# Performance work log

Hardware: AMD Instinct MI355X
Metric: run time of the kernel (lower is better)

The kernel has to match this reference:

```python
import jax, jax.numpy as jnp
import numpy as np

B, L, D, H = 4, 2048, 1024, 16
HD = D // H  # head_dim = 64


def setup_inputs() -> dict:
    key = jax.random.key(0)
    k1, k2, k3 = jax.random.split(key, 3)
    scale_in = 1.0 / np.sqrt(D)
    return {
        "x": jax.random.normal(k1, (B, L, D), dtype=jnp.float32),
        "Wqkv": jax.random.normal(k2, (D, 3 * D), dtype=jnp.float32) * scale_in,
        "Wout": jax.random.normal(k3, (D, D), dtype=jnp.float32) * scale_in,
        "bout": jnp.zeros((D,), dtype=jnp.float32),
    }


def reference(x, Wqkv, Wout, bout):
    b, l, d = x.shape
    # QKV projection (no bias): [B, L, 3D] -> [B, L, 3, H, HD]
    qkv = (x @ Wqkv).reshape(b, l, 3, H, HD)
    q, k, v = jnp.moveaxis(qkv, 2, 0)  # each [B, L, H, HD]
    # scaled scores [B, H, L, L]
    scores = jnp.einsum("blhd,bmhd->bhlm", q, k) / jnp.sqrt(jnp.float32(HD))
    causal_mask = jnp.triu(jnp.ones((l, l), dtype=bool), k=1)
    scores = jnp.where(causal_mask, -jnp.inf, scores)
    attn = jax.nn.softmax(scores, axis=-1)
    # dropout p=0.0 (eval-mode reference) -> identity
    out = jnp.einsum("bhlm,bmhd->blhd", attn, v).reshape(b, l, d)
    return out @ Wout + bout
```

## Files before the change

### kernel.cpp

```cpp
#include <hip/hip_runtime.h>

typedef unsigned short ushort_t;
using bf16x8 = __attribute__((ext_vector_type(8))) short;
using f32x4  = __attribute__((ext_vector_type(4))) float;
using f32x16 = __attribute__((ext_vector_type(16))) float;
using u32x4  = __attribute__((ext_vector_type(4))) unsigned int;

#define B_  4
#define L_  2048
#define D_  1024
#define H_  16
#define HD_ 64
#define N3_ 3072
#define M1_ (B_ * L_)

static __device__ __forceinline__ unsigned short f2bf(float f) {
    unsigned int u = __float_as_uint(f);
    unsigned int r = (u + 0x7fffu + ((u >> 16) & 1u)) >> 16;
    return (unsigned short)r;
}

static __device__ __forceinline__ unsigned int pkbf(float lo, float hi) {
    unsigned int r;
    asm("v_cvt_pk_bf16_f32 %0, %1, %2" : "=v"(r) : "v"(lo), "v"(hi));
    return r;
}

static __device__ __forceinline__ void plswap(unsigned int& a, unsigned int& b) {
    asm volatile("v_permlane32_swap_b32 %0, %1" : "+v"(a), "+v"(b));
}

static __device__ __forceinline__ void async16(const void* g, const void* l) {
    __builtin_amdgcn_global_load_lds(
        (const __attribute__((address_space(1))) void*)g,
        (__attribute__((address_space(3))) void*)l, 16, 0, 0);
}

__global__ void convert_x_kernel(const float4* __restrict__ src,
                                 ushort4* __restrict__ dst) {
    int i = blockIdx.x * blockDim.x + threadIdx.x;
    float4 v = src[i];
    ushort4 o;
    o.x = f2bf(v.x); o.y = f2bf(v.y); o.z = f2bf(v.z); o.w = f2bf(v.w);
    dst[i] = o;
}

__global__ void transpose_conv_kernel(const float* __restrict__ src,
                                      unsigned short* __restrict__ dst,
                                      int rows, int cols) {
    __shared__ float tile[32][33];
    int tx = threadIdx.x, ty = threadIdx.y;
    int c0 = blockIdx.x * 32, r0 = blockIdx.y * 32;
    #pragma unroll
    for (int j = 0; j < 32; j += 8)
        tile[ty + j][tx] = src[(size_t)(r0 + ty + j) * cols + c0 + tx];
    __syncthreads();
    #pragma unroll
    for (int j = 0; j < 32; j += 8)
        dst[(size_t)(c0 + ty + j) * rows + r0 + tx] = f2bf(tile[tx][ty + j]);
}

__global__ __launch_bounds__(512, 2) void gemm256_qkv_kernel(
    const unsigned short* __restrict__ A, const unsigned short* __restrict__ BT,
    unsigned short* __restrict__ qb, unsigned short* __restrict__ kb,
    unsigned short* __restrict__ vb) {
    constexpr int K = 1024, BK = 32, NT = K / BK;
    constexpr int NBX = N3_ / 256;
    constexpr int NWG = (M1_ / 256) * NBX;
    __shared__ __align__(16) unsigned short lds[4][2][256 * BK];

    const int tid = threadIdx.x;
    const int w = tid >> 6, lane = tid & 63;
    const int wr = w >> 2, wc = w & 3;
    const int lg = lane >> 4, ll = lane & 15;

    const int bid = blockIdx.x;
    const int swz = (bid & 7) * (NWG / 8) + (bid >> 3);
    const int m0 = (swz / NBX) * 256, n0 = (swz % NBX) * 256;

    const int srow = w * 16 + (lane >> 2);
    const int scol = (lane & 3) * 8;

    f32x4 acc[8][4] = {};

    #pragma unroll 1
    for (int kt = -3; kt < NT; ++kt) {
        const int ks = kt + 3;
        if (ks < NT) {
            const int buf = ks & 3;
            const size_t koff = (size_t)ks * BK + scol;
            #pragma unroll
            for (int rd = 0; rd < 2; ++rd) {
                async16(&A[(size_t)(m0 + rd * 128 + srow) * K + koff],
                        &lds[buf][0][w * 512 + rd * 4096]);
                async16(&BT[(size_t)(n0 + rd * 128 + srow) * K + koff],
                        &lds[buf][1][w * 512 + rd * 4096]);
            }
        }
        if (kt < 0) continue;

        if (kt == 0) {
            asm volatile("s_waitcnt vmcnt(12)" ::: "memory");
        } else if (kt <= NT - 4) {
            asm volatile("s_waitcnt vmcnt(8)" ::: "memory");
        } else if (kt == NT - 3) {
            asm volatile("s_waitcnt vmcnt(4)" ::: "memory");
        } else {
            asm volatile("s_waitcnt vmcnt(0)" ::: "memory");
        }
        __builtin_amdgcn_s_barrier();
        __builtin_amdgcn_sched_barrier(0);

        const unsigned short* Ab = &lds[kt & 3][0][0];
        const unsigned short* Bb = &lds[kt & 3][1][0];
        bf16x8 af[8], bf[4];
        #pragma unroll
        for (int i = 0; i < 8; ++i)
            af[i] = *(const bf16x8*)&Ab[(wr * 128 + i * 16 + ll) * BK + lg * 8];
        #pragma unroll
        for (int j = 0; j < 4; ++j)
            bf[j] = *(const bf16x8*)&Bb[(wc * 64 + j * 16 + ll) * BK + lg * 8];

        __builtin_amdgcn_s_setprio(1);
        #pragma unroll
        for (int i = 0; i < 8; ++i)
            #pragma unroll
            for (int j = 0; j < 4; ++j)
                acc[i][j] = __builtin_amdgcn_mfma_f32_16x16x32_bf16(
                    af[i], bf[j], acc[i][j], 0, 0, 0);
        __builtin_amdgcn_s_setprio(0);
    }

    #pragma unroll
    for (int mi = 0; mi < 8; ++mi) {
        const int mb = m0 + wr * 128 + mi * 16 + lg * 4;
        #pragma unroll
        for (int ni = 0; ni < 4; ++ni) {
            const int n = n0 + wc * 64 + ni * 16 + ll;
            const int s = n >> 10, h = (n >> 6) & 15, hd = n & 63;
            if (s == 2) {
                const int b = mb >> 11, l = mb & 2047;
                const size_t base = (size_t)(b * H_ + h) * (L_ * HD_);
                ushort4 pk;
                pk.x = f2bf(acc[mi][ni][0]);
                pk.y = f2bf(acc[mi][ni][1]);
                pk.z = f2bf(acc[mi][ni][2]);
                pk.w = f2bf(acc[mi][ni][3]);
                *(ushort4*)&vb[base + (l >> 5) * 2048 + ((l >> 4) & 1) * 1024 +
                               ((l >> 3) & 1) * 512 + hd * 8 + (l & 7)] = pk;
            } else {
                #pragma unroll
                for (int r = 0; r < 4; ++r) {
                    const int m = mb + r;
                    const int b = m >> 11, l = m & 2047;
                    const size_t base = (size_t)(b * H_ + h) * (L_ * HD_);
                    const size_t o = base + (l >> 5) * 2048 + (hd >> 4) * 512 +
                                     ((hd >> 3) & 1) * 256 + (l & 31) * 8 + (hd & 7);
                    unsigned short bv = f2bf(acc[mi][ni][r]);
                    if (s == 0) qb[o] = bv; else kb[o] = bv;
                }
            }
        }
    }
}

__global__ __launch_bounds__(256) void gemm_bt_kernel(
    const unsigned short* __restrict__ A, const unsigned short* __restrict__ BT,
    float* __restrict__ outp, const float* __restrict__ bias) {
    constexpr int K = 1024;
    __shared__ unsigned short As[128 * 32];
    __shared__ unsigned short Bs[128 * 32];
    const int tid = threadIdx.x, w = tid >> 6, lane = tid & 63;
    const int m0 = blockIdx.y * 128, n0 = blockIdx.x * 128;
    const int wm = (w >> 1) * 64, wn = (w & 1) * 64;
    const int lg = lane >> 4, ll = lane & 15;

    f32x4 acc[4][4] = {};

    for (int k0 = 0; k0 < K; k0 += 32) {
        #pragma unroll
        for (int j = 0; j < 2; ++j) {
            int row = w * 32 + j * 16 + (lane >> 2);
            int col = (lane & 3) * 8;
            async16(&A[(size_t)(m0 + row) * K + k0 + col], &As[(w * 32 + j * 16) * 32]);
            async16(&BT[(size_t)(n0 + row) * K + k0 + col], &Bs[(w * 32 + j * 16) * 32]);
        }
        __syncthreads();
        bf16x8 af[4], bfr[4];
        #pragma unroll
        for (int i = 0; i < 4; ++i) {
            af[i]  = *(const bf16x8*)&As[(wm + i * 16 + ll) * 32 + lg * 8];
            bfr[i] = *(const bf16x8*)&Bs[(wn + i * 16 + ll) * 32 + lg * 8];
        }
        #pragma unroll
        for (int mi = 0; mi < 4; ++mi)
            #pragma unroll
            for (int ni = 0; ni < 4; ++ni)
                acc[mi][ni] = __builtin_amdgcn_mfma_f32_16x16x32_bf16(
                    af[mi], bfr[ni], acc[mi][ni], 0, 0, 0);
        __syncthreads();
    }

    #pragma unroll
    for (int mi = 0; mi < 4; ++mi)
        #pragma unroll
        for (int ni = 0; ni < 4; ++ni)
            #pragma unroll
            for (int r = 0; r < 4; ++r) {
                int m = m0 + wm + mi * 16 + lg * 4 + r;
                int n = n0 + wn + ni * 16 + ll;
                outp[(size_t)m * D_ + n] = acc[mi][ni][r] + bias[n];
            }
}

__global__ __launch_bounds__(256) void attn_kernel(
    const unsigned short* __restrict__ qbuf, const unsigned short* __restrict__ kbuf,
    const unsigned short* __restrict__ vbuf, unsigned short* __restrict__ obuf) {
    __shared__ float Sden[4][32];

    const int tid = threadIdx.x;
    const int w = tid >> 6, lane = tid & 63;
    const int lq = lane & 31;
    const int hi = lane >> 5;

    const int bid = blockIdx.x;
    const int grp = bid >> 6;
    const int bh  = bid & 63;
    const int qt  = (15 - grp) * 4 + w;
    const int q0  = qt * 32;

    const unsigned short* Qf = qbuf + (size_t)bh * (L_ * HD_);
    const unsigned short* Kf = kbuf + (size_t)bh * (L_ * HD_);
    const unsigned short* Vf = vbuf + (size_t)bh * (L_ * HD_);

    bf16x8 qf[4];
    #pragma unroll
    for (int c = 0; c < 4; ++c)
        qf[c] = *(const bf16x8*)&Qf[qt * 2048 + c * 512 + hi * 256 + lq * 8];

    f32x16 oa0 = {}, oa1 = {};
    float sden = 0.f;

    const float C1 = 0.18033688011112042f;
    const float C2 = 7.2134752044448165f;

    const int ntiles = qt + 1;

    bf16x8 kf[4];
    #pragma unroll
    for (int c = 0; c < 4; ++c)
        kf[c] = *(const bf16x8*)&Kf[c * 512 + hi * 256 + lq * 8];

    for (int t = 0; t < ntiles; ++t) {
        bf16x8 v0f[2], v1f[2];
        #pragma unroll
        for (int c = 0; c < 2; ++c) {
            v0f[c] = *(const bf16x8*)&Vf[t * 2048 + c * 1024 + hi * 512 + lq * 8];
            v1f[c] = *(const bf16x8*)&Vf[t * 2048 + c * 1024 + hi * 512 + 256 + lq * 8];
        }
        bf16x8 nk[4];
        const bool more = (t + 1 < ntiles);
        if (more) {
            #pragma unroll
            for (int c = 0; c < 4; ++c)
                nk[c] = *(const bf16x8*)&Kf[(t + 1) * 2048 + c * 512 + hi * 256 + lq * 8];
        }

        f32x16 st = {};
        __builtin_amdgcn_s_setprio(1);
        #pragma unroll
        for (int c = 0; c < 4; ++c)
            st = __builtin_amdgcn_mfma_f32_32x32x16_bf16(kf[c], qf[c], st, 0, 0, 0);
        __builtin_amdgcn_s_setprio(0);

        float p[16];
        float rs = 0.f;
        const bool diag = (t == qt);
        #pragma unroll
        for (int r = 0; r < 16; ++r) {
            float pv = exp2f(fmaf(st[r], C1, -C2));
            if (diag) {
                int kv = (r & 3) + 8 * (r >> 2) + 4 * hi;
                if (kv > lq) pv = 0.f;
            }
            p[r] = pv;
            rs += pv;
        }
        rs += __shfl_xor(rs, 32);
        sden += rs;

        unsigned int a0 = pkbf(p[0],  p[1]),  a1 = pkbf(p[2],  p[3]);
        unsigned int b0 = pkbf(p[4],  p[5]),  b1 = pkbf(p[6],  p[7]);
        unsigned int c0 = pkbf(p[8],  p[9]),  c1 = pkbf(p[10], p[11]);
        unsigned int d0 = pkbf(p[12], p[13]), d1 = pkbf(p[14], p[15]);
        plswap(a0, b0);
        plswap(a1, b1);
        plswap(c0, d0);
        plswap(c1, d1);
        u32x4 t0 = {a0, a1, b0, b1};
        u32x4 t1 = {c0, c1, d0, d1};
        bf16x8 pa0 = __builtin_bit_cast(bf16x8, t0);
        bf16x8 pa1 = __builtin_bit_cast(bf16x8, t1);

        __builtin_amdgcn_s_setprio(1);
        oa0 = __builtin_amdgcn_mfma_f32_32x32x16_bf16(pa0, v0f[0], oa0, 0, 0, 0);
        oa1 = __builtin_amdgcn_mfma_f32_32x32x16_bf16(pa0, v1f[0], oa1, 0, 0, 0);
        oa0 = __builtin_amdgcn_mfma_f32_32x32x16_bf16(pa1, v0f[1], oa0, 0, 0, 0);
        oa1 = __builtin_amdgcn_mfma_f32_32x32x16_bf16(pa1, v1f[1], oa1, 0, 0, 0);
        __builtin_amdgcn_s_setprio(0);

        if (more) {
            #pragma unroll
            for (int c = 0; c < 4; ++c) kf[c] = nk[c];
        }
    }

    if (hi == 0) Sden[w][lq] = 1.0f / sden;
    __builtin_amdgcn_s_waitcnt(0);

    const int b = bh >> 4, h = bh & 15;
    #pragma unroll
    for (int r = 0; r < 16; ++r) {
        int q = (r & 3) + 8 * (r >> 2) + 4 * hi;
        float inv = Sden[w][q];
        float o0 = oa0[r] * inv;
        float o1 = oa1[r] * inv;
        size_t row = (size_t)(b * L_ + q0 + q) * D_ + h * HD_;
        obuf[row + lq]      = f2bf(o0);
        obuf[row + 32 + lq] = f2bf(o1);
    }
}

extern "C" void kernel_launch(void* const* d_in, const int* in_sizes, int n_in,
                              void* d_out, int out_size, void* d_ws, size_t ws_size,
                              hipStream_t stream) {
    const float* x    = (const float*)d_in[0];
    const float* Wqkv = (const float*)d_in[1];
    const float* Wout = (const float*)d_in[2];
    const float* bout = (const float*)d_in[3];
    float* out = (float*)d_out;

    char* ws = (char*)d_ws;
    size_t off = 0;
    unsigned short* xb     = (unsigned short*)(ws + off); off += (size_t)M1_ * D_ * 2;
    unsigned short* wqkvT  = (unsigned short*)(ws + off); off += (size_t)N3_ * D_ * 2;
    unsigned short* woutT  = (unsigned short*)(ws + off); off += (size_t)D_ * D_ * 2;
    unsigned short* qb     = (unsigned short*)(ws + off); off += (size_t)B_ * H_ * L_ * HD_ * 2;
    unsigned short* kb     = (unsigned short*)(ws + off); off += (size_t)B_ * H_ * L_ * HD_ * 2;
    unsigned short* vb     = (unsigned short*)(ws + off); off += (size_t)B_ * H_ * L_ * HD_ * 2;
    unsigned short* attnb  = (unsigned short*)(ws + off); off += (size_t)M1_ * D_ * 2;

    convert_x_kernel<<<(M1_ * D_ / 4) / 256, 256, 0, stream>>>(
        (const float4*)x, (ushort4*)xb);
    transpose_conv_kernel<<<dim3(N3_ / 32, D_ / 32), dim3(32, 8), 0, stream>>>(
        Wqkv, wqkvT, D_, N3_);
    transpose_conv_kernel<<<dim3(D_ / 32, D_ / 32), dim3(32, 8), 0, stream>>>(
        Wout, woutT, D_, D_);

    gemm256_qkv_kernel<<<dim3((M1_ / 256) * (N3_ / 256)), 512, 0, stream>>>(
        xb, wqkvT, qb, kb, vb);

    attn_kernel<<<dim3(16 * 64), 256, 0, stream>>>(qb, kb, vb, attnb);

    gemm_bt_kernel<<<dim3(D_ / 128, M1_ / 128), 256, 0, stream>>>(
        attnb, woutT, out, bout);
}
```

Baseline: 188.3 us.

## Swizzle GEMM LDS tiles and double-buffer QKV GEMM for higher occupancy

The QKV GEMM drops from a 4-stage to a 2-stage async-copy ring, halving its LDS footprint. It raises the launch bound from 2 to 4 blocks per CU and adds a trailing barrier so a buffer is not overwritten while it is still being read. Both GEMMs now use an XOR column swizzle on global-to-LDS copies and on fragment reads to cut LDS bank conflicts. The risks: a tighter register cap may spill the 128-float accumulator, and the shallower pipeline exposes more memory latency.

```diff
diff --git a/kernel.cpp b/kernel.cpp
--- a/kernel.cpp
+++ b/kernel.cpp
@@ -60,14 +60,14 @@
         dst[(size_t)(c0 + ty + j) * rows + r0 + tx] = f2bf(tile[tx][ty + j]);
 }
 
-__global__ __launch_bounds__(512, 2) void gemm256_qkv_kernel(
+__global__ __launch_bounds__(512, 4) void gemm256_qkv_kernel(
     const unsigned short* __restrict__ A, const unsigned short* __restrict__ BT,
     unsigned short* __restrict__ qb, unsigned short* __restrict__ kb,
     unsigned short* __restrict__ vb) {
     constexpr int K = 1024, BK = 32, NT = K / BK;
     constexpr int NBX = N3_ / 256;
     constexpr int NWG = (M1_ / 256) * NBX;
-    __shared__ __align__(16) unsigned short lds[4][2][256 * BK];
+    __shared__ __align__(16) unsigned short lds[2][2][256 * BK];
 
     const int tid = threadIdx.x;
     const int w = tid >> 6, lane = tid & 63;
@@ -79,16 +79,24 @@
     const int m0 = (swz / NBX) * 256, n0 = (swz % NBX) * 256;
 
     const int srow = w * 16 + (lane >> 2);
-    const int scol = (lane & 3) * 8;
+    const int scol = (((lane & 3) ^ ((lane >> 3) & 3)) * 8);
+    const int rxor = ((ll >> 1) & 3) * 8;
 
     f32x4 acc[8][4] = {};
 
+    #pragma unroll
+    for (int rd = 0; rd < 2; ++rd) {
+        async16(&A[(size_t)(m0 + rd * 128 + srow) * K + scol],
+                &lds[0][0][w * 512 + rd * 4096]);
+        async16(&BT[(size_t)(n0 + rd * 128 + srow) * K + scol],
+                &lds[0][1][w * 512 + rd * 4096]);
+    }
+
     #pragma unroll 1
-    for (int kt = -3; kt < NT; ++kt) {
-        const int ks = kt + 3;
-        if (ks < NT) {
-            const int buf = ks & 3;
-            const size_t koff = (size_t)ks * BK + scol;
+    for (int kt = 0; kt < NT; ++kt) {
+        if (kt + 1 < NT) {
+            const int buf = (kt + 1) & 1;
+            const size_t koff = (size_t)(kt + 1) * BK + scol;
             #pragma unroll
             for (int rd = 0; rd < 2; ++rd) {
                 async16(&A[(size_t)(m0 + rd * 128 + srow) * K + koff],
@@ -96,14 +104,6 @@
                 async16(&BT[(size_t)(n0 + rd * 128 + srow) * K + koff],
                         &lds[buf][1][w * 512 + rd * 4096]);
             }
-        }
-        if (kt < 0) continue;
-
-        if (kt == 0) {
-            asm volatile("s_waitcnt vmcnt(12)" ::: "memory");
-        } else if (kt <= NT - 4) {
-            asm volatile("s_waitcnt vmcnt(8)" ::: "memory");
-        } else if (kt == NT - 3) {
             asm volatile("s_waitcnt vmcnt(4)" ::: "memory");
         } else {
             asm volatile("s_waitcnt vmcnt(0)" ::: "memory");
@@ -111,15 +111,15 @@
         __builtin_amdgcn_s_barrier();
         __builtin_amdgcn_sched_barrier(0);
 
-        const unsigned short* Ab = &lds[kt & 3][0][0];
-        const unsigned short* Bb = &lds[kt & 3][1][0];
+        const unsigned short* Ab = &lds[kt & 1][0][0];
+        const unsigned short* Bb = &lds[kt & 1][1][0];
         bf16x8 af[8], bf[4];
         #pragma unroll
         for (int i = 0; i < 8; ++i)
-            af[i] = *(const bf16x8*)&Ab[(wr * 128 + i * 16 + ll) * BK + lg * 8];
+            af[i] = *(const bf16x8*)&Ab[(wr * 128 + i * 16 + ll) * BK + (lg * 8 ^ rxor)];
         #pragma unroll
         for (int j = 0; j < 4; ++j)
-            bf[j] = *(const bf16x8*)&Bb[(wc * 64 + j * 16 + ll) * BK + lg * 8];
+            bf[j] = *(const bf16x8*)&Bb[(wc * 64 + j * 16 + ll) * BK + (lg * 8 ^ rxor)];
 
         __builtin_amdgcn_s_setprio(1);
         #pragma unroll
@@ -129,6 +129,7 @@
                 acc[i][j] = __builtin_amdgcn_mfma_f32_16x16x32_bf16(
                     af[i], bf[j], acc[i][j], 0, 0, 0);
         __builtin_amdgcn_s_setprio(0);
+        __builtin_amdgcn_s_barrier();
     }
 
     #pragma unroll
@@ -174,6 +175,8 @@
     const int m0 = blockIdx.y * 128, n0 = blockIdx.x * 128;
     const int wm = (w >> 1) * 64, wn = (w & 1) * 64;
     const int lg = lane >> 4, ll = lane & 15;
+    const int scol = (((lane & 3) ^ ((lane >> 3) & 3)) * 8);
+    const int rxor = ((ll >> 1) & 3) * 8;
 
     f32x4 acc[4][4] = {};
 
@@ -181,16 +184,15 @@
         #pragma unroll
         for (int j = 0; j < 2; ++j) {
             int row = w * 32 + j * 16 + (lane >> 2);
-            int col = (lane & 3) * 8;
-            async16(&A[(size_t)(m0 + row) * K + k0 + col], &As[(w * 32 + j * 16) * 32]);
-            async16(&BT[(size_t)(n0 + row) * K + k0 + col], &Bs[(w * 32 + j * 16) * 32]);
+            async16(&A[(size_t)(m0 + row) * K + k0 + scol], &As[(w * 32 + j * 16) * 32]);
+            async16(&BT[(size_t)(n0 + row) * K + k0 + scol], &Bs[(w * 32 + j * 16) * 32]);
         }
         __syncthreads();
         bf16x8 af[4], bfr[4];
         #pragma unroll
         for (int i = 0; i < 4; ++i) {
-            af[i]  = *(const bf16x8*)&As[(wm + i * 16 + ll) * 32 + lg * 8];
-            bfr[i] = *(const bf16x8*)&Bs[(wn + i * 16 + ll) * 32 + lg * 8];
+            af[i]  = *(const bf16x8*)&As[(wm + i * 16 + ll) * 32 + (lg * 8 ^ rxor)];
+            bfr[i] = *(const bf16x8*)&Bs[(wn + i * 16 + ll) * 32 + (lg * 8 ^ rxor)];
         }
         #pragma unroll
         for (int mi = 0; mi < 4; ++mi)
```

Result: slower. 609.8 us (+223.9%).
